# Kernel optimization log

Measured on AMD Instinct MI355X. Metric: run time of the kernel, lower is better.

Reference implementation:

```python
import jax, jax.numpy as jnp
import numpy as np

N = 50000   # nodes
E = 800000  # edges (avg degree 16)
F = 96      # num_features
H = 96      # hidden_channels
G = 64      # graphs in batch
ALPHA = 0.5


def setup_inputs() -> dict:
    key = jax.random.key(0)
    ks = jax.random.split(key, 32)
    inp = {
        "x": jax.random.normal(ks[0], (N, F), jnp.float32),
        "edge_index": jax.random.randint(ks[1], (2, E), 0, N, dtype=jnp.int32),
        "batch": jnp.sort(jax.random.randint(ks[2], (N,), 0, G, dtype=jnp.int32)),
    }
    i = 3
    dims = [(F, H), (H, H), (H, H)]
    for l, (din, dout) in enumerate(dims, start=1):
        for tag in ("Wself", "Wsd", "Wds"):
            inp[f"{tag}{l}"] = jax.random.normal(ks[i], (din, dout), jnp.float32) * 0.05; i += 1
        for tag in ("bself", "bsd", "bds"):
            inp[f"{tag}{l}"] = jax.random.normal(ks[i], (dout,), jnp.float32) * 0.05; i += 1
    inp["lin1_w"] = jax.random.normal(ks[i], (H, 5), jnp.float32) * 0.05; i += 1
    inp["lin1_b"] = jax.random.normal(ks[i], (5,), jnp.float32) * 0.05; i += 1
    inp["lin2_w"] = jax.random.normal(ks[i], (5, 1), jnp.float32) * 0.05; i += 1
    inp["lin2_b"] = jax.random.normal(ks[i], (1,), jnp.float32) * 0.05
    return inp


def _agg_mean(x, idx_from, idx_to, n):
    # scatter-mean of x[idx_from] onto idx_to (PyG SAGEConv mean aggregation;
    # nodes with no incoming edges get 0)
    s = jax.ops.segment_sum(x[idx_from], idx_to, num_segments=n)
    c = jax.ops.segment_sum(jnp.ones((idx_to.shape[0],), x.dtype), idx_to, num_segments=n)
    return s / jnp.maximum(c, 1.0)[:, None]


def _dir_sage(x, src, dst, Wself, bself, Wsd, bsd, Wds, bds):
    n = x.shape[0]
    out_self = x @ Wself + bself
    # source_to_target: aggregate x[src] at dst; target_to_source: aggregate x[dst] at src
    out_sd = _agg_mean(x, src, dst, n) @ Wsd + bsd
    out_ds = _agg_mean(x, dst, src, n) @ Wds + bds
    return out_self + (1.0 - ALPHA) * out_sd + ALPHA * out_ds


def reference(x, edge_index, batch,
              Wself1, bself1, Wsd1, bsd1, Wds1, bds1,
              Wself2, bself2, Wsd2, bsd2, Wds2, bds2,
              Wself3, bself3, Wsd3, bsd3, Wds3, bds3,
              lin1_w, lin1_b, lin2_w, lin2_b):
    src, dst = edge_index[0], edge_index[1]
    h = jax.nn.relu(_dir_sage(x, src, dst, Wself1, bself1, Wsd1, bsd1, Wds1, bds1))
    h = jax.nn.relu(_dir_sage(h, src, dst, Wself2, bself2, Wsd2, bsd2, Wds2, bds2))
    h = jax.nn.relu(_dir_sage(h, src, dst, Wself3, bself3, Wsd3, bsd3, Wds3, bds3))
    g = jax.ops.segment_max(h, batch, num_segments=G)  # global_max_pool -> [G, H]
    g = jax.nn.relu(g @ lin1_w + lin1_b)
    return g @ lin2_w + lin2_b  # [G, 1]
```

## Files before the change

kernel.cpp:

```cpp
#include <hip/hip_runtime.h>
#include <hip/hip_bf16.h>

#define HF 96
#define GG 64
#define SB 64

typedef __attribute__((ext_vector_type(8))) short bf16x8;
typedef __attribute__((ext_vector_type(4))) float f32x4;

__device__ __forceinline__ unsigned short f2bf(float f) {
    unsigned u = __float_as_uint(f);
    unsigned r = (u + 0x7FFFu + ((u >> 16) & 1u)) >> 16;
    return (unsigned short)r;
}
__device__ __forceinline__ float bf2f(unsigned short h) {
    return __uint_as_float(((unsigned)h) << 16);
}

__global__ void count_kernel(const int* __restrict__ ei, int* __restrict__ cnt_dst,
                             int* __restrict__ cnt_src, int* __restrict__ slot_d,
                             int* __restrict__ slot_s, int E) {
    int e = blockIdx.x * blockDim.x + threadIdx.x;
    if (e >= E) return;
    int s = ei[e];
    int d = ei[E + e];
    slot_d[e] = atomicAdd(&cnt_dst[d], 1);
    slot_s[e] = atomicAdd(&cnt_src[s], 1);
}

__global__ __launch_bounds__(256) void scan_phase1(const int* __restrict__ cnt0,
                                                   const int* __restrict__ cnt1,
                                                   int* __restrict__ off0,
                                                   int* __restrict__ off1,
                                                   int* __restrict__ bsum, int N, int CH) {
    int dir = blockIdx.y;
    const int* cnt = dir ? cnt1 : cnt0;
    int* off = dir ? off1 : off0;
    int base = blockIdx.x * CH;
    int end = base + CH; if (end > N) end = N;
    __shared__ int buf[256];
    int carry = 0;
    for (int s = base; s < end; s += 256) {
        int i = s + threadIdx.x;
        int v = (i < end) ? cnt[i] : 0;
        buf[threadIdx.x] = v;
        __syncthreads();
        for (int st = 1; st < 256; st <<= 1) {
            int tv = (threadIdx.x >= st) ? buf[threadIdx.x - st] : 0;
            __syncthreads();
            buf[threadIdx.x] += tv;
            __syncthreads();
        }
        if (i < end) off[i] = carry + buf[threadIdx.x] - v;
        carry += buf[255];
        __syncthreads();
    }
    if (threadIdx.x == 0) bsum[dir * SB + blockIdx.x] = carry;
}

__global__ __launch_bounds__(64) void scan_phase2(int* __restrict__ bsum, int* __restrict__ boff,
                                                  int* __restrict__ off0, int* __restrict__ off1,
                                                  int N) {
    int dir = blockIdx.x;
    __shared__ int buf[SB];
    int v = bsum[dir * SB + threadIdx.x];
    buf[threadIdx.x] = v;
    __syncthreads();
    for (int st = 1; st < SB; st <<= 1) {
        int tv = (threadIdx.x >= st) ? buf[threadIdx.x - st] : 0;
        __syncthreads();
        buf[threadIdx.x] += tv;
        __syncthreads();
    }
    boff[dir * SB + threadIdx.x] = buf[threadIdx.x] - v;
    if (threadIdx.x == SB - 1) {
        int* off = dir ? off1 : off0;
        off[N] = buf[SB - 1];
    }
}

__global__ void scan_phase3(int* __restrict__ off0, int* __restrict__ off1,
                            const int* __restrict__ boff, int N, int CH) {
    int dir = blockIdx.y;
    int* off = dir ? off1 : off0;
    int i = blockIdx.x * 256 + threadIdx.x;
    if (i >= N) return;
    off[i] += boff[dir * SB + i / CH];
}

__global__ void fill_kernel(const int* __restrict__ ei, const int* __restrict__ off_dst,
                            const int* __restrict__ off_src, const int* __restrict__ slot_d,
                            const int* __restrict__ slot_s, int* __restrict__ nbr_dst,
                            int* __restrict__ nbr_src, int E) {
    int e = blockIdx.x * blockDim.x + threadIdx.x;
    if (e >= E) return;
    int s = ei[e];
    int d = ei[E + e];
    nbr_dst[off_dst[d] + slot_d[e]] = s;
    nbr_src[off_src[s] + slot_s[e]] = d;
}

__global__ void prep_kernel(const float* __restrict__ Wself, const float* __restrict__ Wsd,
                            const float* __restrict__ Wds, const float* __restrict__ bself,
                            const float* __restrict__ bsd, const float* __restrict__ bds,
                            unsigned short* __restrict__ Whi, unsigned short* __restrict__ Wlo,
                            float* __restrict__ bc) {
    int idx = blockIdx.x * 256 + threadIdx.x;
    if (idx < HF * 288) {
        int j = idx / 288;
        int kk = idx % 288;
        int m = kk / HF, k = kk % HF;
        const float* W = (m == 0) ? Wself : (m == 1) ? Wsd : Wds;
        float w = W[k * HF + j];
        unsigned short hi = f2bf(w);
        float rem = w - bf2f(hi);
        Whi[idx] = hi;
        Wlo[idx] = f2bf(rem);
    } else if (idx < HF * 288 + HF) {
        int j = idx - HF * 288;
        bc[j] = bself[j] + 0.5f * (bsd[j] + bds[j]);
    }
}

__global__ __launch_bounds__(256) void gather_kernel(
        const float* __restrict__ x,
        const int* __restrict__ off_dst, const int* __restrict__ nbr_dst,
        const int* __restrict__ off_src, const int* __restrict__ nbr_src,
        float* __restrict__ agg_sd, float* __restrict__ agg_ds, int N) {
    int t = blockIdx.x * blockDim.x + threadIdx.x;
    int n2 = t / 24;
    if (n2 >= 2 * N) return;
    int q = t % 24;
    int dir = (n2 >= N) ? 1 : 0;
    int n = n2 - dir * N;
    const int* off = dir ? off_src : off_dst;
    const int* nbr = dir ? nbr_src : nbr_dst;
    float* agg = dir ? agg_ds : agg_sd;

    int b = off[n], e = off[n + 1];
    const float* xq = x + q * 4;
    float4 a0 = make_float4(0.f, 0.f, 0.f, 0.f);
    float4 a1 = make_float4(0.f, 0.f, 0.f, 0.f);
    float4 a2 = make_float4(0.f, 0.f, 0.f, 0.f);
    float4 a3 = make_float4(0.f, 0.f, 0.f, 0.f);
    int i = b;
    for (; i + 4 <= e; i += 4) {
        int i0 = nbr[i + 0], i1 = nbr[i + 1], i2 = nbr[i + 2], i3 = nbr[i + 3];
        float4 v0 = *(const float4*)(xq + (long long)i0 * HF);
        float4 v1 = *(const float4*)(xq + (long long)i1 * HF);
        float4 v2 = *(const float4*)(xq + (long long)i2 * HF);
        float4 v3 = *(const float4*)(xq + (long long)i3 * HF);
        a0.x += v0.x; a0.y += v0.y; a0.z += v0.z; a0.w += v0.w;
        a1.x += v1.x; a1.y += v1.y; a1.z += v1.z; a1.w += v1.w;
        a2.x += v2.x; a2.y += v2.y; a2.z += v2.z; a2.w += v2.w;
        a3.x += v3.x; a3.y += v3.y; a3.z += v3.z; a3.w += v3.w;
    }
    for (; i < e; i++) {
        int i0 = nbr[i];
        float4 v0 = *(const float4*)(xq + (long long)i0 * HF);
        a0.x += v0.x; a0.y += v0.y; a0.z += v0.z; a0.w += v0.w;
    }
    float4 acc;
    acc.x = (a0.x + a1.x) + (a2.x + a3.x);
    acc.y = (a0.y + a1.y) + (a2.y + a3.y);
    acc.z = (a0.z + a1.z) + (a2.z + a3.z);
    acc.w = (a0.w + a1.w) + (a2.w + a3.w);
    float inv = 0.5f / fmaxf((float)(e - b), 1.0f);
    acc.x *= inv; acc.y *= inv; acc.z *= inv; acc.w *= inv;
    *(float4*)(agg + (long long)n * HF + q * 4) = acc;
}

#define LPAD 40
__global__ __launch_bounds__(256) void sage_mfma(
        const float* __restrict__ x, const float* __restrict__ agg_sd,
        const float* __restrict__ agg_ds,
        const unsigned short* __restrict__ Whi_g, const unsigned short* __restrict__ Wlo_g,
        const float* __restrict__ bc,
        float* __restrict__ out, int N) {
    __shared__ __align__(16) unsigned short Ahi[64 * LPAD];
    __shared__ __align__(16) unsigned short Alo[64 * LPAD];
    __shared__ __align__(16) unsigned short Whi[96 * LPAD];
    __shared__ __align__(16) unsigned short Wlo[96 * LPAD];

    const int tx = threadIdx.x;
    const int lane = tx & 63;
    const int wid = tx >> 6;
    const int wr = (wid >> 1) * 32;
    const int wc = (wid & 1) * 48;
    const int m = lane & 15;
    const int quad = lane >> 4;
    const int row0 = blockIdx.x * 64;

    const int arow = tx >> 2;
    const int aq = tx & 3;
    int argc = row0 + arow; if (argc > N - 1) argc = N - 1;

    f32x4 acc[2][3];
#pragma unroll
    for (int rt = 0; rt < 2; rt++)
#pragma unroll
        for (int ct = 0; ct < 3; ct++) acc[rt][ct] = (f32x4){0.f, 0.f, 0.f, 0.f};

    for (int kt = 0; kt < 9; kt++) {
        const float* A = (kt < 3) ? x : (kt < 6) ? agg_sd : agg_ds;
        const int koff = (kt % 3) * 32;
        const int kglob = kt * 32;

        {
            const float* Ar = A + (long long)argc * HF + koff + aq * 8;
            float4 v0 = *(const float4*)(Ar + 0);
            float4 v1 = *(const float4*)(Ar + 4);
            float f[8] = {v0.x, v0.y, v0.z, v0.w, v1.x, v1.y, v1.z, v1.w};
            bf16x8 hv, lv;
#pragma unroll
            for (int i = 0; i < 8; i++) {
                unsigned short h = f2bf(f[i]);
                hv[i] = (short)h;
                lv[i] = (short)f2bf(f[i] - bf2f(h));
            }
            *(bf16x8*)&Ahi[arow * LPAD + aq * 8] = hv;
            *(bf16x8*)&Alo[arow * LPAD + aq * 8] = lv;
        }
        for (int s = tx; s < 384; s += 256) {
            int n = s >> 2, q2 = s & 3;
            long long go = (long long)n * 288 + kglob + q2 * 8;
            *(bf16x8*)&Whi[n * LPAD + q2 * 8] = *(const bf16x8*)(Whi_g + go);
            *(bf16x8*)&Wlo[n * LPAD + q2 * 8] = *(const bf16x8*)(Wlo_g + go);
        }
        __syncthreads();

        bf16x8 ah[2], al[2], bh[3], bl[3];
#pragma unroll
        for (int rt = 0; rt < 2; rt++) {
            int r = (wr + rt * 16 + m) * LPAD + quad * 8;
            ah[rt] = *(const bf16x8*)&Ahi[r];
            al[rt] = *(const bf16x8*)&Alo[r];
        }
#pragma unroll
        for (int ct = 0; ct < 3; ct++) {
            int r = (wc + ct * 16 + m) * LPAD + quad * 8;
            bh[ct] = *(const bf16x8*)&Whi[r];
            bl[ct] = *(const bf16x8*)&Wlo[r];
        }
#pragma unroll
        for (int rt = 0; rt < 2; rt++)
#pragma unroll
            for (int ct = 0; ct < 3; ct++) {
                acc[rt][ct] = __builtin_amdgcn_mfma_f32_16x16x32_bf16(ah[rt], bh[ct], acc[rt][ct], 0, 0, 0);
                acc[rt][ct] = __builtin_amdgcn_mfma_f32_16x16x32_bf16(ah[rt], bl[ct], acc[rt][ct], 0, 0, 0);
                acc[rt][ct] = __builtin_amdgcn_mfma_f32_16x16x32_bf16(al[rt], bh[ct], acc[rt][ct], 0, 0, 0);
            }
        __syncthreads();
    }

#pragma unroll
    for (int ct = 0; ct < 3; ct++) {
        int col = wc + ct * 16 + m;
        float bcv = bc[col];
#pragma unroll
        for (int rt = 0; rt < 2; rt++) {
#pragma unroll
            for (int reg = 0; reg < 4; reg++) {
                int r = row0 + wr + rt * 16 + quad * 4 + reg;
                if (r < N) out[(long long)r * HF + col] = fmaxf(acc[rt][ct][reg] + bcv, 0.f);
            }
        }
    }
}

#define POOL_CHUNK 128
__global__ void pool_kernel(const float* __restrict__ h, const int* __restrict__ batch,
                            unsigned* __restrict__ g, int N) {
    int j = threadIdx.x;
    if (j >= HF) return;
    int n0 = blockIdx.x * POOL_CHUNK;
    int end = n0 + POOL_CHUNK;
    if (end > N) end = N;
    float cur = 0.0f;
    int curb = -1;
    for (int n = n0; n < end; n++) {
        int b = batch[n];
        float v = h[(long long)n * HF + j];
        if (b != curb) {
            if (curb >= 0) atomicMax(&g[curb * HF + j], __float_as_uint(cur));
            curb = b;
            cur = v;
        } else {
            cur = fmaxf(cur, v);
        }
    }
    if (curb >= 0) atomicMax(&g[curb * HF + j], __float_as_uint(cur));
}

__global__ void mlp_kernel(const unsigned* __restrict__ g, const float* __restrict__ lin1_w,
                           const float* __restrict__ lin1_b, const float* __restrict__ lin2_w,
                           const float* __restrict__ lin2_b, float* __restrict__ out) {
    int gi = threadIdx.x;
    if (gi >= GG) return;
    float h5[5];
#pragma unroll
    for (int hh = 0; hh < 5; hh++) {
        float acc = lin1_b[hh];
#pragma unroll 8
        for (int k = 0; k < HF; k++)
            acc = fmaf(__uint_as_float(g[gi * HF + k]), lin1_w[k * 5 + hh], acc);
        h5[hh] = fmaxf(acc, 0.0f);
    }
    float o = lin2_b[0];
#pragma unroll
    for (int hh = 0; hh < 5; hh++) o = fmaf(h5[hh], lin2_w[hh * 1 + 0], o);
    out[gi] = o;
}

extern "C" void kernel_launch(void* const* d_in, const int* in_sizes, int n_in,
                              void* d_out, int out_size, void* d_ws, size_t ws_size,
                              hipStream_t stream) {
    const float* x     = (const float*)d_in[0];
    const int*   ei    = (const int*)d_in[1];
    const int*   batch = (const int*)d_in[2];
    const float* W[3][3];
    const float* B[3][3];
    for (int l = 0; l < 3; l++) {
        for (int t = 0; t < 3; t++) W[l][t] = (const float*)d_in[3 + l * 6 + t];
        for (int t = 0; t < 3; t++) B[l][t] = (const float*)d_in[3 + l * 6 + 3 + t];
    }
    const float* lin1_w = (const float*)d_in[21];
    const float* lin1_b = (const float*)d_in[22];
    const float* lin2_w = (const float*)d_in[23];
    const float* lin2_b = (const float*)d_in[24];

    const int N = in_sizes[0] / HF;
    const int E = in_sizes[1] / 2;

    float* hA      = (float*)d_ws;
    float* hB      = hA + (long long)N * HF;
    float* agg_sd  = hB + (long long)N * HF;
    float* agg_ds  = agg_sd + (long long)N * HF;
    int*   cnt_dst = (int*)(agg_ds + (long long)N * HF);
    int*   cnt_src = cnt_dst + N;
    int*   off_dst = cnt_src + N;
    int*   off_src = off_dst + (N + 1);
    int*   nbr_dst = off_src + (N + 1);
    int*   nbr_src = nbr_dst + E;
    int*   slot_d  = nbr_src + E;
    int*   slot_s  = slot_d + E;
    int*   bsum    = slot_s + E;
    int*   boff    = bsum + 2 * SB;
    float* bc3     = (float*)(boff + 2 * SB);
    uintptr_t p = (uintptr_t)(bc3 + 3 * HF);
    p = (p + 15) & ~(uintptr_t)15;
    unsigned short* Whi3 = (unsigned short*)p;
    unsigned short* Wlo3 = Whi3 + 3 * HF * 288;
    uintptr_t p2 = (uintptr_t)(Wlo3 + 3 * HF * 288);
    p2 = (p2 + 15) & ~(uintptr_t)15;
    unsigned* g = (unsigned*)p2;

    hipMemsetAsync(cnt_dst, 0, (size_t)2 * N * sizeof(int), stream);
    hipMemsetAsync(g, 0, (size_t)GG * HF * sizeof(unsigned), stream);

    const int prep_blocks = (HF * 288 + HF + 255) / 256;
    for (int l = 0; l < 3; l++)
        prep_kernel<<<prep_blocks, 256, 0, stream>>>(
            W[l][0], W[l][1], W[l][2], B[l][0], B[l][1], B[l][2],
            Whi3 + (long long)l * HF * 288, Wlo3 + (long long)l * HF * 288, bc3 + l * HF);

    const int CH = (N + SB - 1) / SB;
    count_kernel<<<(E + 255) / 256, 256, 0, stream>>>(ei, cnt_dst, cnt_src, slot_d, slot_s, E);
    scan_phase1<<<dim3(SB, 2), 256, 0, stream>>>(cnt_dst, cnt_src, off_dst, off_src, bsum, N, CH);
    scan_phase2<<<2, SB, 0, stream>>>(bsum, boff, off_dst, off_src, N);
    scan_phase3<<<dim3((N + 255) / 256, 2), 256, 0, stream>>>(off_dst, off_src, boff, N, CH);
    fill_kernel<<<(E + 255) / 256, 256, 0, stream>>>(ei, off_dst, off_src,
                                                     slot_d, slot_s, nbr_dst, nbr_src, E);

    const long long gather_threads = (long long)2 * N * 24;
    const int gather_blocks = (int)((gather_threads + 255) / 256);
    const int gemm_blocks = (N + 63) / 64;
    const int pool_blocks = (N + POOL_CHUNK - 1) / POOL_CHUNK;

    const float* cur_in = x;
    float* outs[3] = { hA, hB, hA };
    for (int l = 0; l < 3; l++) {
        gather_kernel<<<gather_blocks, 256, 0, stream>>>(
            cur_in, off_dst, nbr_dst, off_src, nbr_src, agg_sd, agg_ds, N);
        sage_mfma<<<gemm_blocks, 256, 0, stream>>>(
            cur_in, agg_sd, agg_ds,
            Whi3 + (long long)l * HF * 288, Wlo3 + (long long)l * HF * 288,
            bc3 + l * HF, outs[l], N);
        cur_in = outs[l];
    }

    pool_kernel<<<pool_blocks, 128, 0, stream>>>(outs[2], batch, g, N);
    mlp_kernel<<<1, 64, 0, stream>>>(g, lin1_w, lin1_b, lin2_w, lin2_b, (float*)d_out);
}
```

Measured before the change: 561.7 us.

## Fuse neighbor mean-gather into MFMA GEMM kernel via shared-memory aggregates

Merges the gather and GEMM kernels into one per layer. Each block now computes the mean aggregates for its 64 rows in both directions and stores them as bf16 hi/lo pairs in LDS, so agg_sd and agg_ds are never written to or read back from global memory. The gather is restructured so each thread handles 16 features of one row and direction, which gives fewer threads in flight for latency hiding. The larger LDS footprint (about 80KB per block) may also limit occupancy.

```diff
diff --git a/kernel.cpp b/kernel.cpp
--- a/kernel.cpp
+++ b/kernel.cpp
@@ -122,78 +122,107 @@
     }
 }
 
-__global__ __launch_bounds__(256) void gather_kernel(
+#define APAD 200
+#define LPADX 40
+#define LPADW 40
+__global__ __launch_bounds__(256) void sage_fused(
         const float* __restrict__ x,
         const int* __restrict__ off_dst, const int* __restrict__ nbr_dst,
         const int* __restrict__ off_src, const int* __restrict__ nbr_src,
-        float* __restrict__ agg_sd, float* __restrict__ agg_ds, int N) {
-    int t = blockIdx.x * blockDim.x + threadIdx.x;
-    int n2 = t / 24;
-    if (n2 >= 2 * N) return;
-    int q = t % 24;
-    int dir = (n2 >= N) ? 1 : 0;
-    int n = n2 - dir * N;
-    const int* off = dir ? off_src : off_dst;
-    const int* nbr = dir ? nbr_src : nbr_dst;
-    float* agg = dir ? agg_ds : agg_sd;
-
-    int b = off[n], e = off[n + 1];
-    const float* xq = x + q * 4;
-    float4 a0 = make_float4(0.f, 0.f, 0.f, 0.f);
-    float4 a1 = make_float4(0.f, 0.f, 0.f, 0.f);
-    float4 a2 = make_float4(0.f, 0.f, 0.f, 0.f);
-    float4 a3 = make_float4(0.f, 0.f, 0.f, 0.f);
-    int i = b;
-    for (; i + 4 <= e; i += 4) {
-        int i0 = nbr[i + 0], i1 = nbr[i + 1], i2 = nbr[i + 2], i3 = nbr[i + 3];
-        float4 v0 = *(const float4*)(xq + (long long)i0 * HF);
-        float4 v1 = *(const float4*)(xq + (long long)i1 * HF);
-        float4 v2 = *(const float4*)(xq + (long long)i2 * HF);
-        float4 v3 = *(const float4*)(xq + (long long)i3 * HF);
-        a0.x += v0.x; a0.y += v0.y; a0.z += v0.z; a0.w += v0.w;
-        a1.x += v1.x; a1.y += v1.y; a1.z += v1.z; a1.w += v1.w;
-        a2.x += v2.x; a2.y += v2.y; a2.z += v2.z; a2.w += v2.w;
-        a3.x += v3.x; a3.y += v3.y; a3.z += v3.z; a3.w += v3.w;
-    }
-    for (; i < e; i++) {
-        int i0 = nbr[i];
-        float4 v0 = *(const float4*)(xq + (long long)i0 * HF);
-        a0.x += v0.x; a0.y += v0.y; a0.z += v0.z; a0.w += v0.w;
-    }
-    float4 acc;
-    acc.x = (a0.x + a1.x) + (a2.x + a3.x);
-    acc.y = (a0.y + a1.y) + (a2.y + a3.y);
-    acc.z = (a0.z + a1.z) + (a2.z + a3.z);
-    acc.w = (a0.w + a1.w) + (a2.w + a3.w);
-    float inv = 0.5f / fmaxf((float)(e - b), 1.0f);
-    acc.x *= inv; acc.y *= inv; acc.z *= inv; acc.w *= inv;
-    *(float4*)(agg + (long long)n * HF + q * 4) = acc;
-}
-
-#define LPAD 40
-__global__ __launch_bounds__(256) void sage_mfma(
-        const float* __restrict__ x, const float* __restrict__ agg_sd,
-        const float* __restrict__ agg_ds,
         const unsigned short* __restrict__ Whi_g, const unsigned short* __restrict__ Wlo_g,
         const float* __restrict__ bc,
         float* __restrict__ out, int N) {
-    __shared__ __align__(16) unsigned short Ahi[64 * LPAD];
-    __shared__ __align__(16) unsigned short Alo[64 * LPAD];
-    __shared__ __align__(16) unsigned short Whi[96 * LPAD];
-    __shared__ __align__(16) unsigned short Wlo[96 * LPAD];
+    __shared__ __align__(16) unsigned short AggHi[64 * APAD];
+    __shared__ __align__(16) unsigned short AggLo[64 * APAD];
+    __shared__ __align__(16) unsigned short Axhi[64 * LPADX];
+    __shared__ __align__(16) unsigned short Axlo[64 * LPADX];
+    __shared__ __align__(16) unsigned short Wh[96 * LPADW];
+    __shared__ __align__(16) unsigned short Wl[96 * LPADW];
 
     const int tx = threadIdx.x;
+    const int row0 = blockIdx.x * 64;
+
+    for (int it = 0; it < 3; it++) {
+        int task = tx + 256 * it;
+        int row = task & 63;
+        int dir = (task >> 6) & 1;
+        int qg = task >> 7;
+        int r = row0 + row; if (r > N - 1) r = N - 1;
+        const int* off = dir ? off_src : off_dst;
+        const int* nbr = dir ? nbr_src : nbr_dst;
+        int b = off[r], e = off[r + 1];
+        const float* xq = x + qg * 16;
+        float4 a0 = make_float4(0.f,0.f,0.f,0.f), a1 = a0, a2 = a0, a3 = a0;
+        float4 c0 = a0, c1 = a0, c2 = a0, c3 = a0;
+        int i = b;
+        for (; i + 2 <= e; i += 2) {
+            long long r0 = (long long)nbr[i] * HF;
+            long long r1 = (long long)nbr[i + 1] * HF;
+            float4 u0 = *(const float4*)(xq + r0 + 0);
+            float4 u1 = *(const float4*)(xq + r0 + 4);
+            float4 u2 = *(const float4*)(xq + r0 + 8);
+            float4 u3 = *(const float4*)(xq + r0 + 12);
+            float4 w0 = *(const float4*)(xq + r1 + 0);
+            float4 w1 = *(const float4*)(xq + r1 + 4);
+            float4 w2 = *(const float4*)(xq + r1 + 8);
+            float4 w3 = *(const float4*)(xq + r1 + 12);
+            a0.x += u0.x; a0.y += u0.y; a0.z += u0.z; a0.w += u0.w;
+            a1.x += u1.x; a1.y += u1.y; a1.z += u1.z; a1.w += u1.w;
+            a2.x += u2.x; a2.y += u2.y; a2.z += u2.z; a2.w += u2.w;
+            a3.x += u3.x; a3.y += u3.y; a3.z += u3.z; a3.w += u3.w;
+            c0.x += w0.x; c0.y += w0.y; c0.z += w0.z; c0.w += w0.w;
+            c1.x += w1.x; c1.y += w1.y; c1.z += w1.z; c1.w += w1.w;
+            c2.x += w2.x; c2.y += w2.y; c2.z += w2.z; c2.w += w2.w;
+            c3.x += w3.x; c3.y += w3.y; c3.z += w3.z; c3.w += w3.w;
+        }
+        if (i < e) {
+            long long r0 = (long long)nbr[i] * HF;
+            float4 u0 = *(const float4*)(xq + r0 + 0);
+            float4 u1 = *(const float4*)(xq + r0 + 4);
+            float4 u2 = *(const float4*)(xq + r0 + 8);
+            float4 u3 = *(const float4*)(xq + r0 + 12);
+            a0.x += u0.x; a0.y += u0.y; a0.z += u0.z; a0.w += u0.w;
+            a1.x += u1.x; a1.y += u1.y; a1.z += u1.z; a1.w += u1.w;
+            a2.x += u2.x; a2.y += u2.y; a2.z += u2.z; a2.w += u2.w;
+            a3.x += u3.x; a3.y += u3.y; a3.z += u3.z; a3.w += u3.w;
+        }
+        float inv = 0.5f / fmaxf((float)(e - b), 1.0f);
+        float f[16] = {
+            (a0.x + c0.x) * inv, (a0.y + c0.y) * inv, (a0.z + c0.z) * inv, (a0.w + c0.w) * inv,
+            (a1.x + c1.x) * inv, (a1.y + c1.y) * inv, (a1.z + c1.z) * inv, (a1.w + c1.w) * inv,
+            (a2.x + c2.x) * inv, (a2.y + c2.y) * inv, (a2.z + c2.z) * inv, (a2.w + c2.w) * inv,
+            (a3.x + c3.x) * inv, (a3.y + c3.y) * inv, (a3.z + c3.z) * inv, (a3.w + c3.w) * inv };
+        bf16x8 hv0, lv0, hv1, lv1;
+#pragma unroll
+        for (int k = 0; k < 8; k++) {
+            unsigned short h = f2bf(f[k]);
+            hv0[k] = (short)h;
+            lv0[k] = (short)f2bf(f[k] - bf2f(h));
+        }
+#pragma unroll
+        for (int k = 0; k < 8; k++) {
+            unsigned short h = f2bf(f[8 + k]);
+            hv1[k] = (short)h;
+            lv1[k] = (short)f2bf(f[8 + k] - bf2f(h));
+        }
+        int o = row * APAD + dir * 96 + qg * 16;
+        *(bf16x8*)&AggHi[o + 0] = hv0;
+        *(bf16x8*)&AggHi[o + 8] = hv1;
+        *(bf16x8*)&AggLo[o + 0] = lv0;
+        *(bf16x8*)&AggLo[o + 8] = lv1;
+    }
+    __syncthreads();
+
     const int lane = tx & 63;
     const int wid = tx >> 6;
     const int wr = (wid >> 1) * 32;
     const int wc = (wid & 1) * 48;
     const int m = lane & 15;
     const int quad = lane >> 4;
-    const int row0 = blockIdx.x * 64;
 
     const int arow = tx >> 2;
     const int aq = tx & 3;
-    int argc = row0 + arow; if (argc > N - 1) argc = N - 1;
+    int argr = row0 + arow; if (argr > N - 1) argr = N - 1;
 
     f32x4 acc[2][3];
 #pragma unroll
@@ -202,45 +231,52 @@
         for (int ct = 0; ct < 3; ct++) acc[rt][ct] = (f32x4){0.f, 0.f, 0.f, 0.f};
 
     for (int kt = 0; kt < 9; kt++) {
-        const float* A = (kt < 3) ? x : (kt < 6) ? agg_sd : agg_ds;
-        const int koff = (kt % 3) * 32;
         const int kglob = kt * 32;
-
-        {
-            const float* Ar = A + (long long)argc * HF + koff + aq * 8;
+        if (kt < 3) {
+            const float* Ar = x + (long long)argr * HF + (kt * 32) + aq * 8;
             float4 v0 = *(const float4*)(Ar + 0);
             float4 v1 = *(const float4*)(Ar + 4);
             float f[8] = {v0.x, v0.y, v0.z, v0.w, v1.x, v1.y, v1.z, v1.w};
             bf16x8 hv, lv;
 #pragma unroll
-            for (int i = 0; i < 8; i++) {
-                unsigned short h = f2bf(f[i]);
-                hv[i] = (short)h;
-                lv[i] = (short)f2bf(f[i] - bf2f(h));
+            for (int k = 0; k < 8; k++) {
+                unsigned short h = f2bf(f[k]);
+                hv[k] = (short)h;
+                lv[k] = (short)f2bf(f[k] - bf2f(h));
             }
-            *(bf16x8*)&Ahi[arow * LPAD + aq * 8] = hv;
-            *(bf16x8*)&Alo[arow * LPAD + aq * 8] = lv;
+            *(bf16x8*)&Axhi[arow * LPADX + aq * 8] = hv;
+            *(bf16x8*)&Axlo[arow * LPADX + aq * 8] = lv;
         }
         for (int s = tx; s < 384; s += 256) {
-            int n = s >> 2, q2 = s & 3;
-            long long go = (long long)n * 288 + kglob + q2 * 8;
-            *(bf16x8*)&Whi[n * LPAD + q2 * 8] = *(const bf16x8*)(Whi_g + go);
-            *(bf16x8*)&Wlo[n * LPAD + q2 * 8] = *(const bf16x8*)(Wlo_g + go);
+            int j = s >> 2, q2 = s & 3;
+            long long go = (long long)j * 288 + kglob + q2 * 8;
+            *(bf16x8*)&Wh[j * LPADW + q2 * 8] = *(const bf16x8*)(Whi_g + go);
+            *(bf16x8*)&Wl[j * LPADW + q2 * 8] = *(const bf16x8*)(Wlo_g + go);
         }
         __syncthreads();
 
         bf16x8 ah[2], al[2], bh[3], bl[3];
-#pragma unroll
-        for (int rt = 0; rt < 2; rt++) {
-            int r = (wr + rt * 16 + m) * LPAD + quad * 8;
-            ah[rt] = *(const bf16x8*)&Ahi[r];
-            al[rt] = *(const bf16x8*)&Alo[r];
+        if (kt < 3) {
+#pragma unroll
+            for (int rt = 0; rt < 2; rt++) {
+                int r = (wr + rt * 16 + m) * LPADX + quad * 8;
+                ah[rt] = *(const bf16x8*)&Axhi[r];
+                al[rt] = *(const bf16x8*)&Axlo[r];
+            }
+        } else {
+            int kp = (kt - 3) * 32 + quad * 8;
+#pragma unroll
+            for (int rt = 0; rt < 2; rt++) {
+                int r = (wr + rt * 16 + m) * APAD + kp;
+                ah[rt] = *(const bf16x8*)&AggHi[r];
+                al[rt] = *(const bf16x8*)&AggLo[r];
+            }
         }
 #pragma unroll
         for (int ct = 0; ct < 3; ct++) {
-            int r = (wc + ct * 16 + m) * LPAD + quad * 8;
-            bh[ct] = *(const bf16x8*)&Whi[r];
-            bl[ct] = *(const bf16x8*)&Wlo[r];
+            int r = (wc + ct * 16 + m) * LPADW + quad * 8;
+            bh[ct] = *(const bf16x8*)&Wh[r];
+            bl[ct] = *(const bf16x8*)&Wl[r];
         }
 #pragma unroll
         for (int rt = 0; rt < 2; rt++)
@@ -334,9 +370,7 @@
 
     float* hA      = (float*)d_ws;
     float* hB      = hA + (long long)N * HF;
-    float* agg_sd  = hB + (long long)N * HF;
-    float* agg_ds  = agg_sd + (long long)N * HF;
-    int*   cnt_dst = (int*)(agg_ds + (long long)N * HF);
+    int*   cnt_dst = (int*)(hB + (long long)N * HF);
     int*   cnt_src = cnt_dst + N;
     int*   off_dst = cnt_src + N;
     int*   off_src = off_dst + (N + 1);
@@ -372,18 +406,14 @@
     fill_kernel<<<(E + 255) / 256, 256, 0, stream>>>(ei, off_dst, off_src,
                                                      slot_d, slot_s, nbr_dst, nbr_src, E);
 
-    const long long gather_threads = (long long)2 * N * 24;
-    const int gather_blocks = (int)((gather_threads + 255) / 256);
-    const int gemm_blocks = (N + 63) / 64;
+    const int fused_blocks = (N + 63) / 64;
     const int pool_blocks = (N + POOL_CHUNK - 1) / POOL_CHUNK;
 
     const float* cur_in = x;
     float* outs[3] = { hA, hB, hA };
     for (int l = 0; l < 3; l++) {
-        gather_kernel<<<gather_blocks, 256, 0, stream>>>(
-            cur_in, off_dst, nbr_dst, off_src, nbr_src, agg_sd, agg_ds, N);
-        sage_mfma<<<gemm_blocks, 256, 0, stream>>>(
-            cur_in, agg_sd, agg_ds,
+        sage_fused<<<fused_blocks, 256, 0, stream>>>(
+            cur_in, off_dst, nbr_dst, off_src, nbr_src,
             Whi3 + (long long)l * HF * 288, Wlo3 + (long long)l * HF * 288,
             bc3 + l * HF, outs[l], N);
         cur_in = outs[l];
```

Measured after the change: 710.1 us. 1.26x slower.
